# Performance work log

Hardware: AMD Instinct MI355X
Metric: run time of the kernel (lower is better)

## Reference

```python
import jax, jax.numpy as jnp
import numpy as np
from jax import lax

DN = ('NCHW', 'OIHW', 'NCHW')


def setup_inputs() -> dict:
    key = jax.random.key(0)
    ks = jax.random.split(key, 4)
    b, C, H, W = 8, 512, 64, 64
    heads = 8
    return {
        'x': jax.random.normal(ks[0], (b, C, H, W), jnp.float32),
        'qkv_w': jax.random.normal(ks[1], (3 * C, C, 1, 1), jnp.float32) * 0.02,
        'dw_w': jax.random.normal(ks[2], (3 * C, 1, 3, 3), jnp.float32) * 0.02,
        'proj_w': jax.random.normal(ks[3], (C, C, 1, 1), jnp.float32) * 0.02,
        'temperature': jnp.ones((heads, 1, 1), jnp.float32),
        'a1': jnp.full((1,), 0.2, jnp.float32),
        'a2': jnp.full((1,), 0.2, jnp.float32),
        'a3': jnp.full((1,), 0.2, jnp.float32),
        'a4': jnp.full((1,), 0.2, jnp.float32),
    }


def _masked_softmax(attn, k):
    # keep top-k entries per row (same set as torch topk+scatter mask for
    # generic floats), -inf elsewhere, then stable softmax
    thr = lax.top_k(attn, k)[0][..., -1:]
    return jax.nn.softmax(jnp.where(attn >= thr, attn, -jnp.inf), axis=-1)


def _l2norm(t):
    return t / jnp.maximum(jnp.linalg.norm(t, axis=-1, keepdims=True), 1e-12)


def reference(x, qkv_w, dw_w, proj_w, temperature, a1, a2, a3, a4):
    b, c, h, w = x.shape
    heads = temperature.shape[0]
    # 1x1 pointwise conv then 3x3 depthwise conv (groups = 3c)
    qkv = lax.conv_general_dilated(x, qkv_w, (1, 1), 'SAME', dimension_numbers=DN)
    qkv = lax.conv_general_dilated(qkv, dw_w, (1, 1), 'SAME',
                                   feature_group_count=3 * c, dimension_numbers=DN)
    q, k, v = jnp.split(qkv, 3, axis=1)
    # b (head Cph) h w -> b head Cph (h w)
    resh = lambda t: t.reshape(b, heads, c // heads, h * w)
    q, k, v = resh(q), resh(k), resh(v)
    q = _l2norm(q)
    k = _l2norm(k)
    C = q.shape[2]  # channels per head = 64
    attn = jnp.einsum('bhcn,bhdn->bhcd', q, k) * temperature  # (b,heads,C,C)
    out = (_masked_softmax(attn, C // 2) @ v) * a1 \
        + (_masked_softmax(attn, (C * 2) // 3) @ v) * a2 \
        + (_masked_softmax(attn, (C * 3) // 4) @ v) * a3 \
        + (_masked_softmax(attn, (C * 4) // 5) @ v) * a4
    out = out.reshape(b, c, h, w)
    out = lax.conv_general_dilated(out, proj_w, (1, 1), 'SAME', dimension_numbers=DN)
    return out
```

## Files before the change

### kernel.cpp

```cpp
#include <hip/hip_runtime.h>
#include <hip/hip_bf16.h>

#define CHN 512
#define HW  4096
#define C3  1536
#define GB  4

typedef __hip_bfloat16 bf16;
typedef __attribute__((ext_vector_type(8))) short short8;
typedef __attribute__((ext_vector_type(4))) short short4v;
typedef __attribute__((ext_vector_type(4))) float f32x4;
typedef __attribute__((ext_vector_type(4))) int   int4v;
typedef _Float16 h8_t __attribute__((ext_vector_type(8)));

__device__ inline float b2f_bits(short s) {
    union { unsigned u; float f; } uf;
    uf.u = ((unsigned)(unsigned short)s) << 16;
    return uf.f;
}
__device__ inline short f2b_bits(float x) {
    union { __hip_bfloat16 h; short s; } u;
    u.h = __float2bfloat16(x);
    return u.s;
}
__device__ inline void split_bf16(float x, short& hi, short& lo) {
    hi = f2b_bits(x);
    lo = f2b_bits(x - b2f_bits(hi));
}
__device__ inline short f2h_bits(float x) {
    _Float16 h = (_Float16)x;
    return __builtin_bit_cast(short, h);
}
__device__ inline float h2f_bits(short s) {
    return (float)__builtin_bit_cast(_Float16, s);
}
__device__ inline void split_f16(float x, short& hi, short& lo) {
    _Float16 h = (_Float16)x;
    _Float16 l = (_Float16)(x - (float)h);
    hi = __builtin_bit_cast(short, h);
    lo = __builtin_bit_cast(short, l);
}
__device__ inline int swz64(int row, int g) {
    return row * 64 + ((g ^ (row & 7)) << 3);
}
__device__ inline int swz128(int row, int g) {
    return row * 128 + ((g ^ (row & 15)) << 3);
}
__device__ inline void gload16(const void* g, void* l) {
    __builtin_amdgcn_global_load_lds(
        (const __attribute__((address_space(1))) void*)g,
        (__attribute__((address_space(3))) void*)l, 16, 0, 0);
}

__global__ __launch_bounds__(256) void k_w_hi(const float* __restrict__ w,
                                              short* __restrict__ wh, int n4) {
    int i = blockIdx.x * 256 + threadIdx.x;
    if (i < n4) {
        f32x4 v = *(const f32x4*)&w[i * 4];
        short4v h;
#pragma unroll
        for (int j = 0; j < 4; ++j) h[j] = f2h_bits(v[j]);
        *(short4v*)&wh[i * 4] = h;
    }
}

__global__ __launch_bounds__(256) void k_transpose_xf16(const float* __restrict__ in,
                                                        short* __restrict__ out) {
    __shared__ float tile[64][65];
    int b = blockIdx.z;
    int c0 = blockIdx.y * 64, n0 = blockIdx.x * 64;
    const float* ip = in + (long)b * ((long)CHN * HW);
    short* op = out + (long)b * ((long)HW * CHN);
    int t = threadIdx.x;
#pragma unroll
    for (int p = 0; p < 4; ++p) {
        int id = p * 256 + t;
        int r = id >> 4, c4 = (id & 15) * 4;
        f32x4 v = *(const f32x4*)&ip[(long)(c0 + r) * HW + n0 + c4];
#pragma unroll
        for (int j = 0; j < 4; ++j) tile[r][c4 + j] = v[j];
    }
    __syncthreads();
    int col = t & 63, rr = t >> 6;
#pragma unroll
    for (int p = 0; p < 16; ++p) {
        int r = p * 4 + rr;
        op[(long)(n0 + r) * CHN + c0 + col] = f2h_bits(tile[col][r]);
    }
}

template <int MT, bool OUT_F16>
__global__ __launch_bounds__(256) void k_gemm_f16(const short* __restrict__ Ah,
                                                  const short* __restrict__ B,
                                                  void* __restrict__ Cv,
                                                  int M, int N, int K,
                                                  long bB, long bC, long rstride) {
    __shared__ short sAh[MT * 64], sB[128 * 64];
    int b = blockIdx.z;
    int m0 = blockIdx.y * MT, n0 = blockIdx.x * 128;
    const short* Bp = B + (long)b * bB;
    int t = threadIdx.x, wid = t >> 6, lane = t & 63;
    int wr = (wid >> 1) * (MT / 2), wc = (wid & 1) * 64;
    int lrow = lane & 15, khalf = lane >> 4;
    int lrow8 = lane >> 3;
    int gl = ((lane & 7) ^ lrow8) << 3;
    constexpr int MR = MT / 32;
    f32x4 acc[MR][4] = {};
    for (int kt = 0; kt < K; kt += 64) {
#pragma unroll
        for (int i = 0; i < MT / 32; ++i) {
            int rb = i * 32 + wid * 8;
            int row = rb + lrow8;
            gload16(&Ah[(long)(m0 + row) * K + kt + gl], &sAh[rb * 64]);
        }
#pragma unroll
        for (int i = 0; i < 4; ++i) {
            int rb = i * 32 + wid * 8;
            int row = rb + lrow8;
            gload16(&Bp[(long)(n0 + row) * K + kt + gl], &sB[rb * 64]);
        }
        __syncthreads();
#pragma unroll
        for (int ks = 0; ks < 2; ++ks) {
            int gk = ks * 4 + khalf;
            h8_t ah[MR], bh[4];
#pragma unroll
            for (int i = 0; i < MR; ++i)
                ah[i] = *(const h8_t*)&sAh[swz64(wr + i * 16 + lrow, gk)];
#pragma unroll
            for (int i = 0; i < 4; ++i)
                bh[i] = *(const h8_t*)&sB[swz64(wc + i * 16 + lrow, gk)];
#pragma unroll
            for (int mi = 0; mi < MR; ++mi)
#pragma unroll
                for (int ni = 0; ni < 4; ++ni)
                    acc[mi][ni] = __builtin_amdgcn_mfma_f32_16x16x32_f16(
                        ah[mi], bh[ni], acc[mi][ni], 0, 0, 0);
        }
        __syncthreads();
    }
    int crow = (lane >> 4) * 4, ccol = lane & 15;
#pragma unroll
    for (int mi = 0; mi < MR; ++mi)
#pragma unroll
        for (int ni = 0; ni < 4; ++ni)
#pragma unroll
            for (int r = 0; r < 4; ++r) {
                long row = m0 + wr + mi * 16 + crow + r;
                long col = n0 + wc + ni * 16 + ccol;
                float v = acc[mi][ni][r];
                if constexpr (OUT_F16)
                    ((short*)Cv)[(long)b * bC + row * rstride + col] = f2h_bits(v);
                else
                    ((float*)Cv)[(long)b * bC + row * rstride + col] = v;
            }
}

__global__ __launch_bounds__(256) void k_dwl2_rs(int* __restrict__ qkv,
                                                 const float* __restrict__ w) {
    __shared__ float red[4];
    int ch = blockIdx.x, b = blockIdx.y;
    bool is_qk = ch < 1024;
    int* pi = qkv + ((long)b * C3 + ch) * HW;
    short* ps = (short*)pi;
    const short* pin = (const short*)pi;
    float w9[9];
#pragma unroll
    for (int i = 0; i < 9; ++i) w9[i] = w[ch * 9 + i];
    int t = threadIdx.x, wid = t >> 6, lane = t & 63;
    int y0 = wid * 16;
    float out[16];
#pragma unroll
    for (int j = 0; j < 16; ++j) out[j] = 0.f;
#pragma unroll
    for (int i = 0; i < 18; ++i) {
        int r = y0 - 1 + i;
        float v = (r >= 0 && r < 64) ? h2f_bits(pin[r * 64 + lane]) : 0.f;
        float vl = __shfl_up(v, 1);
        float vr = __shfl_down(v, 1);
        if (lane == 0) vl = 0.f;
        if (lane == 63) vr = 0.f;
        int j = i - 1;
        if (j + 1 >= 0 && j + 1 < 16) out[j + 1] += w9[0] * vl + w9[1] * v + w9[2] * vr;
        if (j >= 0 && j < 16)         out[j]     += w9[3] * vl + w9[4] * v + w9[5] * vr;
        if (j - 1 >= 0 && j - 1 < 16) out[j - 1] += w9[6] * vl + w9[7] * v + w9[8] * vr;
    }
    if (is_qk) {
        float ss = 0.f;
#pragma unroll
        for (int j = 0; j < 16; ++j) ss += out[j] * out[j];
#pragma unroll
        for (int o = 32; o; o >>= 1) ss += __shfl_xor(ss, o);
        if (lane == 0) red[wid] = ss;
        __syncthreads();
        float tot = red[0] + red[1] + red[2] + red[3];
        float sc = 1.f / fmaxf(sqrtf(tot), 1e-12f);
#pragma unroll
        for (int j = 0; j < 16; ++j) {
            short hi, lo;
            split_bf16(out[j] * sc, hi, lo);
            int n = (y0 + j) * 64 + lane;
            ps[n] = hi;
            ps[4096 + n] = lo;
        }
    } else {
        __syncthreads();
#pragma unroll
        for (int j = 0; j < 16; ++j)
            ps[(y0 + j) * 64 + lane] = f2h_bits(out[j]);
    }
}

__global__ __launch_bounds__(256) void k_attn_gl(const short* __restrict__ qkv_sh,
                                                 float* __restrict__ attn_part) {
    __shared__ short sQh[64 * 128], sQl[64 * 128], sKh[64 * 128], sKl[64 * 128];
    int h = blockIdx.x, ksl = blockIdx.y, b = blockIdx.z;
    const short* qb = qkv_sh + ((long)b * C3 + h * 64) * (HW * 2L);
    const short* kb = qb + (long)512 * HW * 2;
    int t = threadIdx.x, wid = t >> 6, lane = t & 63;
    int lrow = lane & 15, khalf = lane >> 4;
    f32x4 acc[4] = {};
    for (int kt = ksl * 256; kt < ksl * 256 + 256; kt += 128) {
#pragma unroll
        for (int i = 0; i < 4; ++i) {
            int rb = wid * 16 + i * 4;
            int row = rb + (lane >> 4);
            int gsrc = ((lane & 15) ^ (row & 15)) << 3;
            const short* qrow = qb + (long)row * (HW * 2L) + kt + gsrc;
            const short* krow = kb + (long)row * (HW * 2L) + kt + gsrc;
            gload16(qrow,        &sQh[rb * 128]);
            gload16(qrow + 4096, &sQl[rb * 128]);
            gload16(krow,        &sKh[rb * 128]);
            gload16(krow + 4096, &sKl[rb * 128]);
        }
        __syncthreads();
#pragma unroll
        for (int ks = 0; ks < 4; ++ks) {
            int gk = ks * 4 + khalf;
            short8 kh = *(const short8*)&sKh[swz128(wid * 16 + lrow, gk)];
            short8 kl = *(const short8*)&sKl[swz128(wid * 16 + lrow, gk)];
#pragma unroll
            for (int mi = 0; mi < 4; ++mi) {
                short8 qh = *(const short8*)&sQh[swz128(mi * 16 + lrow, gk)];
                short8 ql = *(const short8*)&sQl[swz128(mi * 16 + lrow, gk)];
                acc[mi] = __builtin_amdgcn_mfma_f32_16x16x32_bf16(qh, kh, acc[mi], 0, 0, 0);
                acc[mi] = __builtin_amdgcn_mfma_f32_16x16x32_bf16(ql, kh, acc[mi], 0, 0, 0);
                acc[mi] = __builtin_amdgcn_mfma_f32_16x16x32_bf16(qh, kl, acc[mi], 0, 0, 0);
            }
        }
        __syncthreads();
    }
    float* op = attn_part + (((long)b * 16 + ksl) * 8 + h) * 4096;
    int crow = (lane >> 4) * 4, ccol = lane & 15;
#pragma unroll
    for (int mi = 0; mi < 4; ++mi)
#pragma unroll
        for (int r = 0; r < 4; ++r)
            op[(mi * 16 + crow + r) * 64 + wid * 16 + ccol] = acc[mi][r];
}

__global__ __launch_bounds__(256) void k_smcomb(const float* __restrict__ attn_part,
                                                const float* __restrict__ temp,
                                                const float* __restrict__ a1,
                                                const float* __restrict__ a2,
                                                const float* __restrict__ a3,
                                                const float* __restrict__ a4,
                                                float* __restrict__ Wc) {
    int t = threadIdx.x, wid = t >> 6, lane = t & 63;
    int b = blockIdx.z;
    int r = blockIdx.x * 4 + wid;
    int h = r >> 6, qr = r & 63;
    float a = 0.f;
#pragma unroll
    for (int s = 0; s < 16; ++s)
        a += attn_part[(((long)b * 16 + s) * 8 + h) * 4096 + qr * 64 + lane];
    a *= temp[h];
    int cnt = 0;
#pragma unroll
    for (int j = 0; j < 64; ++j) {
        float aj = __shfl(a, j);
        cnt += (aj > a) ? 1 : 0;
    }
    float m = a;
#pragma unroll
    for (int o = 32; o; o >>= 1) m = fmaxf(m, __shfl_xor(m, o));
    float e = expf(a - m);
    const int kk[4] = {32, 42, 48, 51};
    float coef[4] = {a1[0], a2[0], a3[0], a4[0]};
    float out = 0.f;
#pragma unroll
    for (int i = 0; i < 4; ++i) {
        float ei = (cnt < kk[i]) ? e : 0.f;
        float d = ei;
#pragma unroll
        for (int o = 32; o; o >>= 1) d += __shfl_xor(d, o);
        out += coef[i] * ei / d;
    }
    Wc[((long)b * 8 + h) * 4096 + qr * 64 + lane] = out;
}

__global__ __launch_bounds__(256) void k_wv_f16(const float* __restrict__ Wc,
                                                const short* __restrict__ qkv_sh,
                                                short* __restrict__ attTs) {
    __shared__ short sVt[128 * 64];
    __shared__ short sWh[64 * 64], sWl[64 * 64];
    int nb = blockIdx.x, h = blockIdx.y, b = blockIdx.z;
    int n0 = nb * 128;
    const float* wp = Wc + ((long)b * 8 + h) * 4096;
    const short* vp = qkv_sh + ((long)b * C3 + 1024 + h * 64) * 8192L;
    int t = threadIdx.x, wid = t >> 6, lane = t & 63;
    int lrow = lane & 15, khalf = lane >> 4;
#pragma unroll
    for (int p = 0; p < 4; ++p) {
        int d = lane;
        int n8 = (p * 4 + wid) * 8;
        short8 v8 = *(const short8*)&vp[(long)d * 8192 + n0 + n8];
#pragma unroll
        for (int j = 0; j < 8; ++j) {
            int n = n8 + j;
            sVt[n * 64 + (((d >> 3) ^ (n & 7)) << 3) + (d & 7)] = v8[j];
        }
    }
#pragma unroll
    for (int p = 0; p < 2; ++p) {
        int id = p * 256 + t, row = id >> 3, g = id & 7;
        f32x4 va = *(const f32x4*)&wp[row * 64 + g * 8];
        f32x4 vb = *(const f32x4*)&wp[row * 64 + g * 8 + 4];
        short8 hh, ll;
#pragma unroll
        for (int j = 0; j < 4; ++j) {
            short h0, l0, h1, l1;
            split_f16(va[j], h0, l0);
            split_f16(vb[j], h1, l1);
            hh[j] = h0;     ll[j] = l0;
            hh[4 + j] = h1; ll[4 + j] = l1;
        }
        int off = swz64(row, g);
        *(short8*)&sWh[off] = hh;
        *(short8*)&sWl[off] = ll;
    }
    __syncthreads();
    f32x4 acc[2][4] = {};
#pragma unroll
    for (int ks = 0; ks < 2; ++ks) {
        int gk = ks * 4 + khalf;
        h8_t vf[2], wh[4], wl[4];
#pragma unroll
        for (int i = 0; i < 2; ++i) {
            int n = wid * 32 + i * 16 + lrow;
            vf[i] = *(const h8_t*)&sVt[n * 64 + ((gk ^ (n & 7)) << 3)];
        }
#pragma unroll
        for (int i = 0; i < 4; ++i) {
            int rr = i * 16 + lrow;
            wh[i] = *(const h8_t*)&sWh[swz64(rr, gk)];
            wl[i] = *(const h8_t*)&sWl[swz64(rr, gk)];
        }
#pragma unroll
        for (int mi = 0; mi < 2; ++mi)
#pragma unroll
            for (int ni = 0; ni < 4; ++ni) {
                acc[mi][ni] = __builtin_amdgcn_mfma_f32_16x16x32_f16(
                    vf[mi], wh[ni], acc[mi][ni], 0, 0, 0);
                acc[mi][ni] = __builtin_amdgcn_mfma_f32_16x16x32_f16(
                    vf[mi], wl[ni], acc[mi][ni], 0, 0, 0);
            }
    }
    short* op = attTs + (long)b * ((long)C3 * HW * 2);
    int crow = (lane >> 4) * 4, ccol = lane & 15;
#pragma unroll
    for (int mi = 0; mi < 2; ++mi)
#pragma unroll
        for (int ni = 0; ni < 4; ++ni)
#pragma unroll
            for (int r = 0; r < 4; ++r) {
                long n = n0 + wid * 32 + mi * 16 + crow + r;
                int c = h * 64 + ni * 16 + ccol;
                op[n * CHN + c] = f2h_bits(acc[mi][ni][r]);
            }
}

extern "C" void kernel_launch(void* const* d_in, const int* in_sizes, int n_in,
                              void* d_out, int out_size, void* d_ws, size_t ws_size,
                              hipStream_t stream) {
    const float* x      = (const float*)d_in[0];
    const float* qkv_w  = (const float*)d_in[1];
    const float* dw_w   = (const float*)d_in[2];
    const float* proj_w = (const float*)d_in[3];
    const float* temp   = (const float*)d_in[4];
    const float* a1     = (const float*)d_in[5];
    const float* a2     = (const float*)d_in[6];
    const float* a3     = (const float*)d_in[7];
    const float* a4     = (const float*)d_in[8];
    float* out = (float*)d_out;

    char* ws = (char*)d_ws;
    int*   qkvi      = (int*)(ws);
    short* xTs       = (short*)(ws + 100663296);
    float* attn_part = (float*)(ws + 100663296);
    float* Wc        = (float*)(ws + 138412032);
    short* wph       = (short*)(ws + 138936320);
    short* wqh       = (short*)(ws + 139460608);

    k_w_hi<<<256, 256, 0, stream>>>(proj_w, wph, 65536);
    k_w_hi<<<768, 256, 0, stream>>>(qkv_w, wqh, 196608);

    for (int g = 0; g < 2; ++g) {
        const float* xg = x + (long)g * GB * CHN * HW;
        float* outg = out + (long)g * GB * CHN * HW;
        k_transpose_xf16<<<dim3(64, 8, GB), 256, 0, stream>>>(xg, xTs);
        k_gemm_f16<128, true><<<dim3(32, 12, GB), 256, 0, stream>>>(
            wqh, xTs, qkvi, C3, HW, CHN,
            (long)HW * CHN, (long)C3 * 8192, 8192);
        k_dwl2_rs<<<dim3(C3, GB), 256, 0, stream>>>(qkvi, dw_w);
        k_attn_gl<<<dim3(8, 16, GB), 256, 0, stream>>>((const short*)qkvi, attn_part);
        k_smcomb<<<dim3(128, 1, GB), 256, 0, stream>>>(attn_part, temp, a1, a2, a3, a4, Wc);
        k_wv_f16<<<dim3(32, 8, GB), 256, 0, stream>>>(Wc, (const short*)qkvi, (short*)qkvi);
        k_gemm_f16<64, false><<<dim3(32, 8, GB), 256, 0, stream>>>(
            wph, (const short*)qkvi, outg, CHN, HW, CHN,
            (long)C3 * HW * 2, (long)CHN * HW, HW);
    }
}
```

Before: 260.5 us.

## Use single fp16 Q/K in attention GEMM instead of split bf16 hi/lo

The depthwise+L2-norm kernel now writes the normalized Q and K as one fp16 value instead of a bf16 hi/lo pair. The Q·K^T attention kernel then loads half as much data into shared memory and issues one f16 MFMA per tile instead of three bf16 MFMAs. The two weight-conversion launches are also merged into a single kernel. This trades accuracy of the attention logits, which feed a top-k threshold mask, for less memory traffic and matrix work. Near-tie top-k selections could flip as a result.

Result: faster. 247.5 us (-5.0%).

```diff
diff --git a/kernel.cpp b/kernel.cpp
--- a/kernel.cpp
+++ b/kernel.cpp
@@ -13,20 +13,6 @@
 typedef __attribute__((ext_vector_type(4))) int   int4v;
 typedef _Float16 h8_t __attribute__((ext_vector_type(8)));
 
-__device__ inline float b2f_bits(short s) {
-    union { unsigned u; float f; } uf;
-    uf.u = ((unsigned)(unsigned short)s) << 16;
-    return uf.f;
-}
-__device__ inline short f2b_bits(float x) {
-    union { __hip_bfloat16 h; short s; } u;
-    u.h = __float2bfloat16(x);
-    return u.s;
-}
-__device__ inline void split_bf16(float x, short& hi, short& lo) {
-    hi = f2b_bits(x);
-    lo = f2b_bits(x - b2f_bits(hi));
-}
 __device__ inline short f2h_bits(float x) {
     _Float16 h = (_Float16)x;
     return __builtin_bit_cast(short, h);
@@ -52,16 +38,21 @@
         (__attribute__((address_space(3))) void*)l, 16, 0, 0);
 }
 
-__global__ __launch_bounds__(256) void k_w_hi(const float* __restrict__ w,
-                                              short* __restrict__ wh, int n4) {
+__global__ __launch_bounds__(256) void k_w_hi2(const float* __restrict__ wp_,
+                                               short* __restrict__ wph,
+                                               const float* __restrict__ wq_,
+                                               short* __restrict__ wqh) {
     int i = blockIdx.x * 256 + threadIdx.x;
-    if (i < n4) {
-        f32x4 v = *(const f32x4*)&w[i * 4];
-        short4v h;
-#pragma unroll
-        for (int j = 0; j < 4; ++j) h[j] = f2h_bits(v[j]);
-        *(short4v*)&wh[i * 4] = h;
-    }
+    const float* src;
+    short* dst;
+    int j;
+    if (i < 65536) { src = wp_; dst = wph; j = i; }
+    else           { src = wq_; dst = wqh; j = i - 65536; }
+    f32x4 v = *(const f32x4*)&src[j * 4];
+    short4v h;
+#pragma unroll
+    for (int k = 0; k < 4; ++k) h[k] = f2h_bits(v[k]);
+    *(short4v*)&dst[j * 4] = h;
 }
 
 __global__ __launch_bounds__(256) void k_transpose_xf16(const float* __restrict__ in,
@@ -156,14 +147,12 @@
             }
 }
 
-__global__ __launch_bounds__(256) void k_dwl2_rs(int* __restrict__ qkv,
+__global__ __launch_bounds__(256) void k_dwl2_rs(short* __restrict__ qkv,
                                                  const float* __restrict__ w) {
     __shared__ float red[4];
     int ch = blockIdx.x, b = blockIdx.y;
     bool is_qk = ch < 1024;
-    int* pi = qkv + ((long)b * C3 + ch) * HW;
-    short* ps = (short*)pi;
-    const short* pin = (const short*)pi;
+    short* ps = qkv + ((long)b * C3 + ch) * 8192L;
     float w9[9];
 #pragma unroll
     for (int i = 0; i < 9; ++i) w9[i] = w[ch * 9 + i];
@@ -175,7 +164,7 @@
 #pragma unroll
     for (int i = 0; i < 18; ++i) {
         int r = y0 - 1 + i;
-        float v = (r >= 0 && r < 64) ? h2f_bits(pin[r * 64 + lane]) : 0.f;
+        float v = (r >= 0 && r < 64) ? h2f_bits(ps[r * 64 + lane]) : 0.f;
         float vl = __shfl_up(v, 1);
         float vr = __shfl_down(v, 1);
         if (lane == 0) vl = 0.f;
@@ -185,6 +174,7 @@
         if (j >= 0 && j < 16)         out[j]     += w9[3] * vl + w9[4] * v + w9[5] * vr;
         if (j - 1 >= 0 && j - 1 < 16) out[j - 1] += w9[6] * vl + w9[7] * v + w9[8] * vr;
     }
+    float sc = 1.f;
     if (is_qk) {
         float ss = 0.f;
 #pragma unroll
@@ -194,29 +184,21 @@
         if (lane == 0) red[wid] = ss;
         __syncthreads();
         float tot = red[0] + red[1] + red[2] + red[3];
-        float sc = 1.f / fmaxf(sqrtf(tot), 1e-12f);
-#pragma unroll
-        for (int j = 0; j < 16; ++j) {
-            short hi, lo;
-            split_bf16(out[j] * sc, hi, lo);
-            int n = (y0 + j) * 64 + lane;
-            ps[n] = hi;
-            ps[4096 + n] = lo;
-        }
+        sc = 1.f / fmaxf(sqrtf(tot), 1e-12f);
     } else {
         __syncthreads();
-#pragma unroll
-        for (int j = 0; j < 16; ++j)
-            ps[(y0 + j) * 64 + lane] = f2h_bits(out[j]);
-    }
+    }
+#pragma unroll
+    for (int j = 0; j < 16; ++j)
+        ps[(y0 + j) * 64 + lane] = f2h_bits(out[j] * sc);
 }
 
 __global__ __launch_bounds__(256) void k_attn_gl(const short* __restrict__ qkv_sh,
                                                  float* __restrict__ attn_part) {
-    __shared__ short sQh[64 * 128], sQl[64 * 128], sKh[64 * 128], sKl[64 * 128];
+    __shared__ short sQ[64 * 128], sK[64 * 128];
     int h = blockIdx.x, ksl = blockIdx.y, b = blockIdx.z;
-    const short* qb = qkv_sh + ((long)b * C3 + h * 64) * (HW * 2L);
-    const short* kb = qb + (long)512 * HW * 2;
+    const short* qb = qkv_sh + ((long)b * C3 + h * 64) * 8192L;
+    const short* kb = qb + (long)512 * 8192;
     int t = threadIdx.x, wid = t >> 6, lane = t & 63;
     int lrow = lane & 15, khalf = lane >> 4;
     f32x4 acc[4] = {};
@@ -226,26 +208,18 @@
             int rb = wid * 16 + i * 4;
             int row = rb + (lane >> 4);
             int gsrc = ((lane & 15) ^ (row & 15)) << 3;
-            const short* qrow = qb + (long)row * (HW * 2L) + kt + gsrc;
-            const short* krow = kb + (long)row * (HW * 2L) + kt + gsrc;
-            gload16(qrow,        &sQh[rb * 128]);
-            gload16(qrow + 4096, &sQl[rb * 128]);
-            gload16(krow,        &sKh[rb * 128]);
-            gload16(krow + 4096, &sKl[rb * 128]);
+            gload16(qb + (long)row * 8192 + kt + gsrc, &sQ[rb * 128]);
+            gload16(kb + (long)row * 8192 + kt + gsrc, &sK[rb * 128]);
         }
         __syncthreads();
 #pragma unroll
         for (int ks = 0; ks < 4; ++ks) {
             int gk = ks * 4 + khalf;
-            short8 kh = *(const short8*)&sKh[swz128(wid * 16 + lrow, gk)];
-            short8 kl = *(const short8*)&sKl[swz128(wid * 16 + lrow, gk)];
+            h8_t kf = *(const h8_t*)&sK[swz128(wid * 16 + lrow, gk)];
 #pragma unroll
             for (int mi = 0; mi < 4; ++mi) {
-                short8 qh = *(const short8*)&sQh[swz128(mi * 16 + lrow, gk)];
-                short8 ql = *(const short8*)&sQl[swz128(mi * 16 + lrow, gk)];
-                acc[mi] = __builtin_amdgcn_mfma_f32_16x16x32_bf16(qh, kh, acc[mi], 0, 0, 0);
-                acc[mi] = __builtin_amdgcn_mfma_f32_16x16x32_bf16(ql, kh, acc[mi], 0, 0, 0);
-                acc[mi] = __builtin_amdgcn_mfma_f32_16x16x32_bf16(qh, kl, acc[mi], 0, 0, 0);
+                h8_t qf = *(const h8_t*)&sQ[swz128(mi * 16 + lrow, gk)];
+                acc[mi] = __builtin_amdgcn_mfma_f32_16x16x32_f16(qf, kf, acc[mi], 0, 0, 0);
             }
         }
         __syncthreads();
@@ -395,15 +369,14 @@
     float* out = (float*)d_out;
 
     char* ws = (char*)d_ws;
-    int*   qkvi      = (int*)(ws);
+    short* qkvi      = (short*)(ws);
     short* xTs       = (short*)(ws + 100663296);
     float* attn_part = (float*)(ws + 100663296);
     float* Wc        = (float*)(ws + 138412032);
     short* wph       = (short*)(ws + 138936320);
     short* wqh       = (short*)(ws + 139460608);
 
-    k_w_hi<<<256, 256, 0, stream>>>(proj_w, wph, 65536);
-    k_w_hi<<<768, 256, 0, stream>>>(qkv_w, wqh, 196608);
+    k_w_hi2<<<1024, 256, 0, stream>>>(proj_w, wph, qkv_w, wqh);
 
     for (int g = 0; g < 2; ++g) {
         const float* xg = x + (long)g * GB * CHN * HW;
@@ -413,11 +386,11 @@
             wqh, xTs, qkvi, C3, HW, CHN,
             (long)HW * CHN, (long)C3 * 8192, 8192);
         k_dwl2_rs<<<dim3(C3, GB), 256, 0, stream>>>(qkvi, dw_w);
-        k_attn_gl<<<dim3(8, 16, GB), 256, 0, stream>>>((const short*)qkvi, attn_part);
+        k_attn_gl<<<dim3(8, 16, GB), 256, 0, stream>>>(qkvi, attn_part);
         k_smcomb<<<dim3(128, 1, GB), 256, 0, stream>>>(attn_part, temp, a1, a2, a3, a4, Wc);
-        k_wv_f16<<<dim3(32, 8, GB), 256, 0, stream>>>(Wc, (const short*)qkvi, (short*)qkvi);
+        k_wv_f16<<<dim3(32, 8, GB), 256, 0, stream>>>(Wc, qkvi, qkvi);
         k_gemm_f16<64, false><<<dim3(32, 8, GB), 256, 0, stream>>>(
-            wph, (const short*)qkvi, outg, CHN, HW, CHN,
+            wph, qkvi, outg, CHN, HW, CHN,
             (long)C3 * HW * 2, (long)CHN * HW, HW);
     }
 }
```
